# Performance work log

Measured on AMD Instinct MI355X. Metric: run time of the kernel, lower is better.

## Reference

```python
import jax, jax.numpy as jnp
import numpy as np

B, N, D = 4, 2048, 768
OUT = 768

def setup_inputs() -> dict:
    key = jax.random.key(0)
    k1, k2 = jax.random.split(key)
    x = jax.random.normal(k1, (B, N, D), dtype=jnp.float32)
    kernel = jax.random.normal(k2, (3, D, OUT), dtype=jnp.float32) * 0.02
    return {"x": x, "kernel": kernel}

def reference(x, kernel):
    # Single-head attention with shared QKV kernel stack [3, D, OUT]
    q = jnp.einsum('bnd,do->bno', x, kernel[0])
    k = jnp.einsum('bnd,do->bno', x, kernel[1])
    v = jnp.einsum('bnd,do->bno', x, kernel[2])
    # NOTE: original divides by 64**0.5 == 8 regardless of dims (faithful)
    scores = jnp.einsum('bqo,bko->bqk', q, k) / 8.0
    attn = jax.nn.softmax(scores, axis=-1)
    return jnp.einsum('bqk,bko->bqo', attn, v)
```

## Files before the change

### kernel.cpp

```cpp
#include <hip/hip_runtime.h>
#include <hip/hip_bf16.h>

constexpr int B_ = 4, N_ = 2048, D_ = 768, OUT_ = 768;
constexpr int M_ = B_ * N_;

typedef __attribute__((ext_vector_type(8))) short short8;
typedef __attribute__((ext_vector_type(4))) float floatx4;

__device__ __forceinline__ unsigned short f2bfu(float f) {
    union { __hip_bfloat16 b; unsigned short u; } cv;
    cv.b = __float2bfloat16(f);
    return cv.u;
}

#define GLOAD_LDS16(g, l)                                                     \
    __builtin_amdgcn_global_load_lds(                                         \
        (const __attribute__((address_space(1))) void*)(g),                   \
        (__attribute__((address_space(3))) void*)(l), 16, 0, 0)

#define MFMA_BF16 __builtin_amdgcn_mfma_f32_16x16x32_bf16
#define SBAR __builtin_amdgcn_s_barrier
#define SCHED0 __builtin_amdgcn_sched_barrier

template <int MFR, int NT>
__device__ __forceinline__ void gemm_tb(
    const __hip_bfloat16* __restrict__ aG, int lda,
    const __hip_bfloat16* __restrict__ bG, int ldb,
    unsigned short* LDS, floatx4 (&acc)[MFR][4]) {
    constexpr int BSLOT = (MFR == 4) ? 8192 : 4096;
    constexpr int BUFS = 4096 + BSLOT;
    constexpr int LOADS = (MFR == 4) ? 3 : 2;
    const int tid = threadIdx.x;
    const int wave = tid >> 6, lane = tid & 63;
    const int lr = lane & 15, kq = lane >> 4;
    const int wm = (MFR == 4) ? (wave >> 2) * 64 : (wave >> 1) * 32;
    const int wn = (MFR == 4) ? (wave & 3) * 64 : (wave & 1) * 64;

    const int p0 = tid >> 3, g0 = (tid & 7) ^ (p0 & 7);
    const __hip_bfloat16* pa =
        aG + (size_t)(2 * p0 + (g0 >> 2)) * lda + (g0 & 3) * 8;
    const __hip_bfloat16* pb0 =
        bG + (size_t)(2 * p0 + (g0 >> 2)) * ldb + (g0 & 3) * 8;
    const __hip_bfloat16* pb1 = bG;
    if constexpr (MFR == 4) {
        const int u = 512 + tid, p1 = u >> 3, g1 = (u & 7) ^ (p1 & 7);
        pb1 = bG + (size_t)(2 * p1 + (g1 >> 2)) * ldb + (g1 & 3) * 8;
    }

    int oa[MFR], ob[4];
#pragma unroll
    for (int mi = 0; mi < MFR; ++mi) {
        const int r = wm + mi * 16 + lr, p = r >> 1;
        const int g = ((r & 1) << 2) | kq;
        oa[mi] = p * 64 + ((g ^ (p & 7)) * 8);
    }
#pragma unroll
    for (int ni = 0; ni < 4; ++ni) {
        const int r = wn + ni * 16 + lr, p = r >> 1;
        const int g = ((r & 1) << 2) | kq;
        ob[ni] = p * 64 + ((g ^ (p & 7)) * 8);
    }

    auto STAGE = [&](int tt, int buf) {
        unsigned short* d = LDS + buf * BUFS + wave * 512;
        GLOAD_LDS16(pa + tt * 32, d);
        GLOAD_LDS16(pb0 + tt * 32, d + 4096);
        if constexpr (MFR == 4) GLOAD_LDS16(pb1 + tt * 32, d + 8192);
    };

    STAGE(0, 0);
    STAGE(1, 1);
    asm volatile("s_waitcnt vmcnt(%0)" ::"i"(LOADS) : "memory");
    SBAR();
    SCHED0(0);

    int bR = 0, bS = 2;
    for (int t = 0; t < NT; ++t) {
        const unsigned short* Ab = LDS + bR * BUFS;
        const unsigned short* Bb = Ab + 4096;
        short8 af[MFR], bf[4];
#pragma unroll
        for (int mi = 0; mi < MFR; ++mi)
            af[mi] = *(const short8*)(Ab + oa[mi]);
#pragma unroll
        for (int ni = 0; ni < 4; ++ni)
            bf[ni] = *(const short8*)(Bb + ob[ni]);
        if (t + 2 < NT) STAGE(t + 2, bS);
#pragma unroll
        for (int mi = 0; mi < MFR; ++mi)
#pragma unroll
            for (int ni = 0; ni < 4; ++ni)
                acc[mi][ni] = MFMA_BF16(af[mi], bf[ni], acc[mi][ni], 0, 0, 0);
        if (t + 2 < NT)
            asm volatile("s_waitcnt vmcnt(%0)" ::"i"(LOADS) : "memory");
        else if (t + 1 < NT)
            asm volatile("s_waitcnt vmcnt(0)" ::: "memory");
        if (t + 1 < NT) {
            SBAR();
            SCHED0(0);
        }
        bR = (bR == 2) ? 0 : bR + 1;
        bS = (bS == 2) ? 0 : bS + 1;
    }
}

__global__ __launch_bounds__(256)
void prep(const float* __restrict__ x, const float* __restrict__ w,
          __hip_bfloat16* __restrict__ xb, __hip_bfloat16* __restrict__ wt,
          float* __restrict__ l) {
    __shared__ float t[32][33];
    const int tid = threadIdx.x;
    if (blockIdx.x < 3072) {
        const size_t i = (size_t)blockIdx.x * 2048 + (size_t)tid * 8;
        float4 a = *(const float4*)(x + i);
        float4 b = *(const float4*)(x + i + 4);
        *(ushort4*)((unsigned short*)xb + i) =
            make_ushort4(f2bfu(a.x), f2bfu(a.y), f2bfu(a.z), f2bfu(a.w));
        *(ushort4*)((unsigned short*)xb + i + 4) =
            make_ushort4(f2bfu(b.x), f2bfu(b.y), f2bfu(b.z), f2bfu(b.w));
    } else if (blockIdx.x < 4800) {
        const int bid = blockIdx.x - 3072;
        const int s = bid / 576, rem = bid % 576;
        const int d0 = (rem / 24) * 32, o0 = (rem % 24) * 32;
        const int tx = tid & 31, ty = tid >> 5;
        const float* ws = w + (size_t)s * D_ * OUT_;
        __hip_bfloat16* wts = wt + (size_t)s * OUT_ * D_;
#pragma unroll
        for (int i = 0; i < 4; ++i)
            t[ty + 8 * i][tx] = ws[(size_t)(d0 + ty + 8 * i) * OUT_ + o0 + tx];
        __syncthreads();
#pragma unroll
        for (int i = 0; i < 4; ++i)
            wts[(size_t)(o0 + ty + 8 * i) * D_ + d0 + tx] =
                __float2bfloat16(t[tx][ty + 8 * i]);
    } else {
        float4* l4 = (float4*)l;
#pragma unroll
        for (int i = 0; i < 8; ++i) l4[i * 256 + tid] = make_float4(0, 0, 0, 0);
    }
}

__global__ __launch_bounds__(512, 4)
void qkv_mfma(const __hip_bfloat16* __restrict__ xb,
              const __hip_bfloat16* __restrict__ wt,
              __hip_bfloat16* __restrict__ q, __hip_bfloat16* __restrict__ k,
              __hip_bfloat16* __restrict__ vt) {
    __shared__ __align__(16) unsigned short LDS[36864];
    const int s = blockIdx.z;
    const int m0 = blockIdx.x * 128, n0 = blockIdx.y * 256;
    floatx4 acc[4][4] = {};
    gemm_tb<4, 24>(xb + (size_t)m0 * D_, D_,
                   wt + (size_t)s * OUT_ * D_ + (size_t)n0 * D_, D_, LDS, acc);

    const int tid = threadIdx.x, wave = tid >> 6, lane = tid & 63;
    const int lrow = lane & 15, kq = lane >> 4;
    const int wm = (wave >> 2) * 64, wn = (wave & 3) * 64;
    unsigned short* E = LDS;

    if (s < 2) {
        __syncthreads();
#pragma unroll
        for (int mi = 0; mi < 4; ++mi)
#pragma unroll
            for (int ni = 0; ni < 4; ++ni) {
                const int n = wn + ni * 16 + lrow;
#pragma unroll
                for (int r = 0; r < 4; ++r)
                    E[(wm + mi * 16 + kq * 4 + r) * 264 + n] =
                        f2bfu(acc[mi][ni][r]);
            }
        __syncthreads();
        unsigned short* outp = (unsigned short*)(s == 0 ? q : k);
#pragma unroll
        for (int i = 0; i < 8; ++i) {
            const int u = i * 512 + tid, row = u >> 5, c = u & 31;
            *(short8*)(outp + (size_t)(m0 + row) * OUT_ + n0 + c * 8) =
                *(const short8*)(E + row * 264 + c * 8);
        }
    } else {
        __syncthreads();
#pragma unroll
        for (int mi = 0; mi < 4; ++mi)
#pragma unroll
            for (int ni = 0; ni < 4; ++ni) {
                const int n = wn + ni * 16 + lrow;
#pragma unroll
                for (int r = 0; r < 4; ++r)
                    E[n * 136 + wm + mi * 16 + kq * 4 + r] =
                        f2bfu(acc[mi][ni][r]);
            }
        __syncthreads();
        const int b = m0 >> 11, j0 = m0 & 2047;
#pragma unroll
        for (int i = 0; i < 8; ++i) {
            const int u = i * 512 + tid, nr = u >> 4, c = u & 15;
            *(short8*)((unsigned short*)vt + ((size_t)b * OUT_ + n0 + nr) * N_ +
                       j0 + c * 8) = *(const short8*)(E + nr * 136 + c * 8);
        }
    }
}

__global__ __launch_bounds__(512, 4)
void scores_mfma(const __hip_bfloat16* __restrict__ q,
                 const __hip_bfloat16* __restrict__ k,
                 __hip_bfloat16* __restrict__ pt, float* __restrict__ l) {
    __shared__ __align__(16) unsigned short LDS[36864];
    const int b = blockIdx.z;
    const int m0 = blockIdx.x * 128, n0 = blockIdx.y * 256;
    floatx4 acc[4][4] = {};
    gemm_tb<4, 24>(q + (size_t)b * N_ * OUT_ + (size_t)m0 * OUT_, OUT_,
                   k + (size_t)b * N_ * OUT_ + (size_t)n0 * OUT_, OUT_, LDS,
                   acc);

    const int tid = threadIdx.x, wave = tid >> 6, lane = tid & 63;
    const int lrow = lane & 15, kq = lane >> 4;
    const int wm = (wave >> 2) * 64, wn = (wave & 3) * 64;

    float rs[4][4];
#pragma unroll
    for (int mi = 0; mi < 4; ++mi)
#pragma unroll
        for (int r = 0; r < 4; ++r) rs[mi][r] = 0.0f;
#pragma unroll
    for (int mi = 0; mi < 4; ++mi)
#pragma unroll
        for (int ni = 0; ni < 4; ++ni)
#pragma unroll
            for (int r = 0; r < 4; ++r) {
                const float e = __expf(acc[mi][ni][r] * 0.125f - 8.0f);
                acc[mi][ni][r] = e;
                rs[mi][r] += e;
            }
#pragma unroll
    for (int mi = 0; mi < 4; ++mi)
#pragma unroll
        for (int r = 0; r < 4; ++r) {
            float v = rs[mi][r];
            v += __shfl_xor(v, 1, 64);
            v += __shfl_xor(v, 2, 64);
            v += __shfl_xor(v, 4, 64);
            v += __shfl_xor(v, 8, 64);
            if (lrow == 0)
                atomicAdd(&l[(size_t)b * N_ + m0 + wm + mi * 16 + kq * 4 + r],
                          v);
        }

    unsigned short* E = LDS;
    unsigned short* pb = (unsigned short*)pt + (size_t)b * N_ * N_;
    __syncthreads();
#pragma unroll
    for (int mi = 0; mi < 4; ++mi)
#pragma unroll
        for (int ni = 0; ni < 4; ++ni) {
            const int n = wn + ni * 16 + lrow;
#pragma unroll
            for (int r = 0; r < 4; ++r)
                E[(wm + mi * 16 + kq * 4 + r) * 258 + n] =
                    f2bfu(acc[mi][ni][r]);
        }
    __syncthreads();
#pragma unroll
    for (int i = 0; i < 8; ++i) {
        const int u = i * 512 + tid, row = u >> 5, c = u & 31;
        *(short8*)(pb + (size_t)(m0 + row) * N_ + n0 + c * 8) =
            *(const short8*)(E + row * 258 + c * 8);
    }
}

__global__ __launch_bounds__(512, 4)
void pv_mfma(const __hip_bfloat16* __restrict__ pt,
             const __hip_bfloat16* __restrict__ vt,
             const float* __restrict__ l, float* __restrict__ out) {
    __shared__ __align__(16) unsigned short LDS[24576];
    const int b = blockIdx.z;
    const int m0 = blockIdx.x * 128, n0 = blockIdx.y * 128;
    floatx4 acc[2][4] = {};
    gemm_tb<2, 64>(pt + (size_t)b * N_ * N_ + (size_t)m0 * N_, N_,
                   vt + (size_t)b * OUT_ * N_ + (size_t)n0 * N_, N_, LDS, acc);

    const int tid = threadIdx.x, wave = tid >> 6, lane = tid & 63;
    const int lrow = lane & 15, kq = lane >> 4;
    const int wm = (wave >> 1) * 32, wn = (wave & 1) * 64;
    const float* lb = l + (size_t)b * N_ + m0 + wm;
#pragma unroll
    for (int mi = 0; mi < 2; ++mi)
#pragma unroll
        for (int r = 0; r < 4; ++r) {
            const float inv = 1.0f / lb[mi * 16 + kq * 4 + r];
            float* o = out +
                       ((size_t)b * N_ + m0 + wm + mi * 16 + kq * 4 + r) *
                           OUT_ +
                       n0 + wn;
#pragma unroll
            for (int ni = 0; ni < 4; ++ni)
                o[ni * 16 + lrow] = acc[mi][ni][r] * inv;
        }
}

extern "C" void kernel_launch(void* const* d_in, const int* in_sizes, int n_in,
                              void* d_out, int out_size, void* d_ws,
                              size_t ws_size, hipStream_t stream) {
    const float* x = (const float*)d_in[0];
    const float* w = (const float*)d_in[1];
    float* out = (float*)d_out;

    __hip_bfloat16* q  = (__hip_bfloat16*)d_ws;
    __hip_bfloat16* k  = q + (size_t)M_ * OUT_;
    __hip_bfloat16* vt = k + (size_t)M_ * OUT_;
    __hip_bfloat16* xb = vt + (size_t)M_ * OUT_;
    __hip_bfloat16* wt = xb + (size_t)M_ * D_;
    float* l = (float*)(wt + (size_t)3 * OUT_ * D_);
    __hip_bfloat16* pt = (__hip_bfloat16*)(l + M_);

    prep<<<dim3(4801), dim3(256), 0, stream>>>(x, w, xb, wt, l);
    qkv_mfma<<<dim3(64, 3, 3), dim3(512), 0, stream>>>(xb, wt, q, k, vt);
    scores_mfma<<<dim3(16, 8, 4), dim3(512), 0, stream>>>(q, k, pt, l);
    pv_mfma<<<dim3(16, 6, 4), dim3(512), 0, stream>>>(pt, vt, l, out);
}
```

Before: 189.7 us.

## Switch GEMMs to double-buffered LDS, halve epilogue staging, retile PV kernel

Replaces the triple-buffered LDS pipeline with a double-buffered one that issues the next tile's loads before the current tile's MFMAs, and raises MFMA wave priority with s_setprio. Epilogues now stage output in two halves so each kernel needs less LDS, which allows six blocks per CU instead of four in the QKV and scores kernels. The PV kernel moves to 256-thread blocks with 64x256 tiles and a 4x4 accumulator per wave. The aim is more resident waves to hide latency, at the cost of shallower prefetch and an extra barrier pair in each epilogue.

```diff
diff --git a/kernel.cpp b/kernel.cpp
--- a/kernel.cpp
+++ b/kernel.cpp
@@ -21,86 +21,79 @@
 #define MFMA_BF16 __builtin_amdgcn_mfma_f32_16x16x32_bf16
 #define SBAR __builtin_amdgcn_s_barrier
 #define SCHED0 __builtin_amdgcn_sched_barrier
-
-template <int MFR, int NT>
-__device__ __forceinline__ void gemm_tb(
+#define PRIO __builtin_amdgcn_s_setprio
+
+template <int THREADS, int NT>
+__device__ __forceinline__ void gemm_db(
     const __hip_bfloat16* __restrict__ aG, int lda,
     const __hip_bfloat16* __restrict__ bG, int ldb,
-    unsigned short* LDS, floatx4 (&acc)[MFR][4]) {
-    constexpr int BSLOT = (MFR == 4) ? 8192 : 4096;
-    constexpr int BUFS = 4096 + BSLOT;
-    constexpr int LOADS = (MFR == 4) ? 3 : 2;
+    unsigned short* LDS, floatx4 (&acc)[4][4]) {
+    constexpr int NB = (THREADS == 512) ? 2 : 4;
+    constexpr int BBASE = (THREADS == 512) ? 4096 : 2048;
+    constexpr int BUFS = BBASE + 8192;
     const int tid = threadIdx.x;
     const int wave = tid >> 6, lane = tid & 63;
     const int lr = lane & 15, kq = lane >> 4;
-    const int wm = (MFR == 4) ? (wave >> 2) * 64 : (wave >> 1) * 32;
-    const int wn = (MFR == 4) ? (wave & 3) * 64 : (wave & 1) * 64;
+    const int wm = (THREADS == 512) ? (wave >> 2) * 64 : 0;
+    const int wn = (THREADS == 512) ? (wave & 3) * 64 : wave * 64;
 
     const int p0 = tid >> 3, g0 = (tid & 7) ^ (p0 & 7);
     const __hip_bfloat16* pa =
         aG + (size_t)(2 * p0 + (g0 >> 2)) * lda + (g0 & 3) * 8;
-    const __hip_bfloat16* pb0 =
-        bG + (size_t)(2 * p0 + (g0 >> 2)) * ldb + (g0 & 3) * 8;
-    const __hip_bfloat16* pb1 = bG;
-    if constexpr (MFR == 4) {
-        const int u = 512 + tid, p1 = u >> 3, g1 = (u & 7) ^ (p1 & 7);
-        pb1 = bG + (size_t)(2 * p1 + (g1 >> 2)) * ldb + (g1 & 3) * 8;
-    }
-
-    int oa[MFR], ob[4];
-#pragma unroll
-    for (int mi = 0; mi < MFR; ++mi) {
-        const int r = wm + mi * 16 + lr, p = r >> 1;
-        const int g = ((r & 1) << 2) | kq;
-        oa[mi] = p * 64 + ((g ^ (p & 7)) * 8);
-    }
-#pragma unroll
-    for (int ni = 0; ni < 4; ++ni) {
-        const int r = wn + ni * 16 + lr, p = r >> 1;
-        const int g = ((r & 1) << 2) | kq;
-        ob[ni] = p * 64 + ((g ^ (p & 7)) * 8);
+    const __hip_bfloat16* pb[NB];
+#pragma unroll
+    for (int j = 0; j < NB; ++j) {
+        const int u = j * THREADS + tid, p = u >> 3, g = (u & 7) ^ (p & 7);
+        pb[j] = bG + (size_t)(2 * p + (g >> 2)) * ldb + (g & 3) * 8;
+    }
+
+    int oa[4], ob[4];
+#pragma unroll
+    for (int i = 0; i < 4; ++i) {
+        const int ra = wm + i * 16 + lr, pA = ra >> 1;
+        const int gA = ((ra & 1) << 2) | kq;
+        oa[i] = pA * 64 + ((gA ^ (pA & 7)) * 8);
+        const int rb = wn + i * 16 + lr, pB = rb >> 1;
+        const int gB = ((rb & 1) << 2) | kq;
+        ob[i] = pB * 64 + ((gB ^ (pB & 7)) * 8);
     }
 
     auto STAGE = [&](int tt, int buf) {
         unsigned short* d = LDS + buf * BUFS + wave * 512;
         GLOAD_LDS16(pa + tt * 32, d);
-        GLOAD_LDS16(pb0 + tt * 32, d + 4096);
-        if constexpr (MFR == 4) GLOAD_LDS16(pb1 + tt * 32, d + 8192);
+#pragma unroll
+        for (int j = 0; j < NB; ++j)
+            GLOAD_LDS16(pb[j] + tt * 32, d + BBASE + j * (THREADS * 8));
     };
 
     STAGE(0, 0);
-    STAGE(1, 1);
-    asm volatile("s_waitcnt vmcnt(%0)" ::"i"(LOADS) : "memory");
+    asm volatile("s_waitcnt vmcnt(0)" ::: "memory");
     SBAR();
     SCHED0(0);
 
-    int bR = 0, bS = 2;
     for (int t = 0; t < NT; ++t) {
-        const unsigned short* Ab = LDS + bR * BUFS;
-        const unsigned short* Bb = Ab + 4096;
-        short8 af[MFR], bf[4];
-#pragma unroll
-        for (int mi = 0; mi < MFR; ++mi)
+        if (t + 1 < NT) STAGE(t + 1, (t + 1) & 1);
+        const unsigned short* Ab = LDS + (t & 1) * BUFS;
+        const unsigned short* Bb = Ab + BBASE;
+        short8 af[4], bf[4];
+#pragma unroll
+        for (int mi = 0; mi < 4; ++mi)
             af[mi] = *(const short8*)(Ab + oa[mi]);
 #pragma unroll
         for (int ni = 0; ni < 4; ++ni)
             bf[ni] = *(const short8*)(Bb + ob[ni]);
-        if (t + 2 < NT) STAGE(t + 2, bS);
-#pragma unroll
-        for (int mi = 0; mi < MFR; ++mi)
+        PRIO(1);
+#pragma unroll
+        for (int mi = 0; mi < 4; ++mi)
 #pragma unroll
             for (int ni = 0; ni < 4; ++ni)
                 acc[mi][ni] = MFMA_BF16(af[mi], bf[ni], acc[mi][ni], 0, 0, 0);
-        if (t + 2 < NT)
-            asm volatile("s_waitcnt vmcnt(%0)" ::"i"(LOADS) : "memory");
-        else if (t + 1 < NT)
+        PRIO(0);
+        if (t + 1 < NT) {
             asm volatile("s_waitcnt vmcnt(0)" ::: "memory");
-        if (t + 1 < NT) {
             SBAR();
             SCHED0(0);
         }
-        bR = (bR == 2) ? 0 : bR + 1;
-        bS = (bS == 2) ? 0 : bS + 1;
     }
 }
 
@@ -140,17 +133,18 @@
     }
 }
 
-__global__ __launch_bounds__(512, 4)
+__global__ __launch_bounds__(512, 6)
 void qkv_mfma(const __hip_bfloat16* __restrict__ xb,
               const __hip_bfloat16* __restrict__ wt,
               __hip_bfloat16* __restrict__ q, __hip_bfloat16* __restrict__ k,
               __hip_bfloat16* __restrict__ vt) {
-    __shared__ __align__(16) unsigned short LDS[36864];
+    __shared__ __align__(16) unsigned short LDS[24576];
     const int s = blockIdx.z;
     const int m0 = blockIdx.x * 128, n0 = blockIdx.y * 256;
     floatx4 acc[4][4] = {};
-    gemm_tb<4, 24>(xb + (size_t)m0 * D_, D_,
-                   wt + (size_t)s * OUT_ * D_ + (size_t)n0 * D_, D_, LDS, acc);
+    gemm_db<512, 24>(xb + (size_t)m0 * D_, D_,
+                     wt + (size_t)s * OUT_ * D_ + (size_t)n0 * D_, D_, LDS,
+                     acc);
 
     const int tid = threadIdx.x, wave = tid >> 6, lane = tid & 63;
     const int lrow = lane & 15, kq = lane >> 4;
@@ -158,59 +152,70 @@
     unsigned short* E = LDS;
 
     if (s < 2) {
-        __syncthreads();
-#pragma unroll
-        for (int mi = 0; mi < 4; ++mi)
-#pragma unroll
-            for (int ni = 0; ni < 4; ++ni) {
-                const int n = wn + ni * 16 + lrow;
-#pragma unroll
-                for (int r = 0; r < 4; ++r)
-                    E[(wm + mi * 16 + kq * 4 + r) * 264 + n] =
-                        f2bfu(acc[mi][ni][r]);
-            }
-        __syncthreads();
         unsigned short* outp = (unsigned short*)(s == 0 ? q : k);
 #pragma unroll
-        for (int i = 0; i < 8; ++i) {
-            const int u = i * 512 + tid, row = u >> 5, c = u & 31;
-            *(short8*)(outp + (size_t)(m0 + row) * OUT_ + n0 + c * 8) =
-                *(const short8*)(E + row * 264 + c * 8);
+        for (int h = 0; h < 2; ++h) {
+            __syncthreads();
+            if ((wave >> 2) == h) {
+#pragma unroll
+                for (int mi = 0; mi < 4; ++mi)
+#pragma unroll
+                    for (int ni = 0; ni < 4; ++ni) {
+                        const int n = wn + ni * 16 + lrow;
+#pragma unroll
+                        for (int r = 0; r < 4; ++r)
+                            E[(mi * 16 + kq * 4 + r) * 264 + n] =
+                                f2bfu(acc[mi][ni][r]);
+                    }
+            }
+            __syncthreads();
+#pragma unroll
+            for (int i = 0; i < 4; ++i) {
+                const int u = i * 512 + tid, row = u >> 5, c = u & 31;
+                *(short8*)(outp + (size_t)(m0 + h * 64 + row) * OUT_ + n0 +
+                           c * 8) = *(const short8*)(E + row * 264 + c * 8);
+            }
         }
     } else {
-        __syncthreads();
-#pragma unroll
-        for (int mi = 0; mi < 4; ++mi)
-#pragma unroll
-            for (int ni = 0; ni < 4; ++ni) {
-                const int n = wn + ni * 16 + lrow;
-#pragma unroll
-                for (int r = 0; r < 4; ++r)
-                    E[n * 136 + wm + mi * 16 + kq * 4 + r] =
-                        f2bfu(acc[mi][ni][r]);
-            }
-        __syncthreads();
         const int b = m0 >> 11, j0 = m0 & 2047;
 #pragma unroll
-        for (int i = 0; i < 8; ++i) {
-            const int u = i * 512 + tid, nr = u >> 4, c = u & 15;
-            *(short8*)((unsigned short*)vt + ((size_t)b * OUT_ + n0 + nr) * N_ +
-                       j0 + c * 8) = *(const short8*)(E + nr * 136 + c * 8);
-        }
-    }
-}
-
-__global__ __launch_bounds__(512, 4)
+        for (int h = 0; h < 2; ++h) {
+            __syncthreads();
+            if ((wn >> 7) == h) {
+#pragma unroll
+                for (int mi = 0; mi < 4; ++mi)
+#pragma unroll
+                    for (int ni = 0; ni < 4; ++ni) {
+                        const int nl = (wn & 127) + ni * 16 + lrow;
+#pragma unroll
+                        for (int r = 0; r < 4; ++r)
+                            E[nl * 136 + wm + mi * 16 + kq * 4 + r] =
+                                f2bfu(acc[mi][ni][r]);
+                    }
+            }
+            __syncthreads();
+#pragma unroll
+            for (int i = 0; i < 4; ++i) {
+                const int u = i * 512 + tid, nr = u >> 4, c = u & 15;
+                *(short8*)((unsigned short*)vt +
+                           ((size_t)b * OUT_ + n0 + h * 128 + nr) * N_ + j0 +
+                           c * 8) = *(const short8*)(E + nr * 136 + c * 8);
+            }
+        }
+    }
+}
+
+__global__ __launch_bounds__(512, 6)
 void scores_mfma(const __hip_bfloat16* __restrict__ q,
                  const __hip_bfloat16* __restrict__ k,
                  __hip_bfloat16* __restrict__ pt, float* __restrict__ l) {
-    __shared__ __align__(16) unsigned short LDS[36864];
+    __shared__ __align__(16) unsigned short LDS[24576];
     const int b = blockIdx.z;
     const int m0 = blockIdx.x * 128, n0 = blockIdx.y * 256;
     floatx4 acc[4][4] = {};
-    gemm_tb<4, 24>(q + (size_t)b * N_ * OUT_ + (size_t)m0 * OUT_, OUT_,
-                   k + (size_t)b * N_ * OUT_ + (size_t)n0 * OUT_, OUT_, LDS,
-                   acc);
+    gemm_db<512, 24>(q + (size_t)b * N_ * OUT_ + (size_t)m0 * OUT_, OUT_,
+                     k + (size_t)b * N_ * OUT_ + (size_t)n0 * OUT_, OUT_, LDS,
+                     acc);
 
     const int tid = threadIdx.x, wave = tid >> 6, lane = tid & 63;
     const int lrow = lane & 15, kq = lane >> 4;
@@ -247,50 +252,55 @@
 
     unsigned short* E = LDS;
     unsigned short* pb = (unsigned short*)pt + (size_t)b * N_ * N_;
-    __syncthreads();
-#pragma unroll
-    for (int mi = 0; mi < 4; ++mi)
-#pragma unroll
-        for (int ni = 0; ni < 4; ++ni) {
-            const int n = wn + ni * 16 + lrow;
-#pragma unroll
-            for (int r = 0; r < 4; ++r)
-                E[(wm + mi * 16 + kq * 4 + r) * 258 + n] =
-                    f2bfu(acc[mi][ni][r]);
-        }
-    __syncthreads();
-#pragma unroll
-    for (int i = 0; i < 8; ++i) {
-        const int u = i * 512 + tid, row = u >> 5, c = u & 31;
-        *(short8*)(pb + (size_t)(m0 + row) * N_ + n0 + c * 8) =
-            *(const short8*)(E + row * 258 + c * 8);
-    }
-}
-
-__global__ __launch_bounds__(512, 4)
+#pragma unroll
+    for (int h = 0; h < 2; ++h) {
+        __syncthreads();
+        if ((wave >> 2) == h) {
+#pragma unroll
+            for (int mi = 0; mi < 4; ++mi)
+#pragma unroll
+                for (int ni = 0; ni < 4; ++ni) {
+                    const int n = wn + ni * 16 + lrow;
+#pragma unroll
+                    for (int r = 0; r < 4; ++r)
+                        E[(mi * 16 + kq * 4 + r) * 258 + n] =
+                            f2bfu(acc[mi][ni][r]);
+                }
+        }
+        __syncthreads();
+#pragma unroll
+        for (int i = 0; i < 4; ++i) {
+            const int u = i * 512 + tid, row = u >> 5, c = u & 31;
+            *(short8*)(pb + (size_t)(m0 + h * 64 + row) * N_ + n0 + c * 8) =
+                *(const short8*)(E + row * 258 + c * 8);
+        }
+    }
+}
+
+__global__ __launch_bounds__(256, 4)
 void pv_mfma(const __hip_bfloat16* __restrict__ pt,
              const __hip_bfloat16* __restrict__ vt,
              const float* __restrict__ l, float* __restrict__ out) {
-    __shared__ __align__(16) unsigned short LDS[24576];
+    __shared__ __align__(16) unsigned short LDS[20480];
     const int b = blockIdx.z;
-    const int m0 = blockIdx.x * 128, n0 = blockIdx.y * 128;
-    floatx4 acc[2][4] = {};
-    gemm_tb<2, 64>(pt + (size_t)b * N_ * N_ + (size_t)m0 * N_, N_,
-                   vt + (size_t)b * OUT_ * N_ + (size_t)n0 * N_, N_, LDS, acc);
+    const int m0 = blockIdx.x * 64, n0 = blockIdx.y * 256;
+    floatx4 acc[4][4] = {};
+    gemm_db<256, 64>(pt + (size_t)b * N_ * N_ + (size_t)m0 * N_, N_,
+                     vt + (size_t)b * OUT_ * N_ + (size_t)n0 * N_, N_, LDS,
+                     acc);
 
     const int tid = threadIdx.x, wave = tid >> 6, lane = tid & 63;
     const int lrow = lane & 15, kq = lane >> 4;
-    const int wm = (wave >> 1) * 32, wn = (wave & 1) * 64;
-    const float* lb = l + (size_t)b * N_ + m0 + wm;
-#pragma unroll
-    for (int mi = 0; mi < 2; ++mi)
+    const int wn = wave * 64;
+    const float* lb = l + (size_t)b * N_ + m0;
+#pragma unroll
+    for (int mi = 0; mi < 4; ++mi)
 #pragma unroll
         for (int r = 0; r < 4; ++r) {
-            const float inv = 1.0f / lb[mi * 16 + kq * 4 + r];
-            float* o = out +
-                       ((size_t)b * N_ + m0 + wm + mi * 16 + kq * 4 + r) *
-                           OUT_ +
-                       n0 + wn;
+            const int row = mi * 16 + kq * 4 + r;
+            const float inv = 1.0f / lb[row];
+            float* o =
+                out + ((size_t)b * N_ + m0 + row) * OUT_ + n0 + wn;
 #pragma unroll
             for (int ni = 0; ni < 4; ++ni)
                 o[ni * 16 + lrow] = acc[mi][ni][r] * inv;
@@ -315,5 +325,5 @@
     prep<<<dim3(4801), dim3(256), 0, stream>>>(x, w, xb, wt, l);
     qkv_mfma<<<dim3(64, 3, 3), dim3(512), 0, stream>>>(xb, wt, q, k, vt);
     scores_mfma<<<dim3(16, 8, 4), dim3(512), 0, stream>>>(q, k, pt, l);
-    pv_mfma<<<dim3(16, 6, 4), dim3(512), 0, stream>>>(pt, vt, l, out);
-}
+    pv_mfma<<<dim3(32, 3, 4), dim3(256), 0, stream>>>(pt, vt, l, out);
+}
```

Measured after the change: 527.7 us. 178% more time.

## Use 256x256 block tiles with split-phase MFMA pipeline for QKV and scores GEMMs

Applied to the files above, without the earlier changes.

The QKV and scores GEMMs move from 128x256 to 256x256 block tiles, with each wave computing a 128x64 sub-tile. The main loop is split into two MFMA phases that interleave the A and B global-to-LDS stages, and it raises wave priority with s_setprio around the MFMA bursts. The aim is to cut global and LDS traffic per FLOP and overlap loads with math better. In exchange the accumulators double, occupancy drops to 2 blocks per SM, and the grids shrink to 288 and 256 blocks, which may underfill the 256 CUs.

```diff
diff --git a/kernel.cpp b/kernel.cpp
--- a/kernel.cpp
+++ b/kernel.cpp
@@ -21,56 +21,149 @@
 #define MFMA_BF16 __builtin_amdgcn_mfma_f32_16x16x32_bf16
 #define SBAR __builtin_amdgcn_s_barrier
 #define SCHED0 __builtin_amdgcn_sched_barrier
-
-template <int MFR, int NT>
-__device__ __forceinline__ void gemm_tb(
+#define PRIO __builtin_amdgcn_s_setprio
+#define WAIT_LGKM0 asm volatile("s_waitcnt lgkmcnt(0)" ::: "memory")
+
+template <int NT>
+__device__ __forceinline__ void gemm8p(
     const __hip_bfloat16* __restrict__ aG, int lda,
     const __hip_bfloat16* __restrict__ bG, int ldb,
-    unsigned short* LDS, floatx4 (&acc)[MFR][4]) {
-    constexpr int BSLOT = (MFR == 4) ? 8192 : 4096;
-    constexpr int BUFS = 4096 + BSLOT;
-    constexpr int LOADS = (MFR == 4) ? 3 : 2;
+    unsigned short* LDS, floatx4 (&acc)[8][4]) {
     const int tid = threadIdx.x;
     const int wave = tid >> 6, lane = tid & 63;
     const int lr = lane & 15, kq = lane >> 4;
-    const int wm = (MFR == 4) ? (wave >> 2) * 64 : (wave >> 1) * 32;
-    const int wn = (MFR == 4) ? (wave & 3) * 64 : (wave & 1) * 64;
+    const int wm = (wave >> 2) * 128, wn = (wave & 3) * 64;
 
     const int p0 = tid >> 3, g0 = (tid & 7) ^ (p0 & 7);
     const __hip_bfloat16* pa =
         aG + (size_t)(2 * p0 + (g0 >> 2)) * lda + (g0 & 3) * 8;
-    const __hip_bfloat16* pb0 =
+    const __hip_bfloat16* pb =
         bG + (size_t)(2 * p0 + (g0 >> 2)) * ldb + (g0 & 3) * 8;
-    const __hip_bfloat16* pb1 = bG;
-    if constexpr (MFR == 4) {
-        const int u = 512 + tid, p1 = u >> 3, g1 = (u & 7) ^ (p1 & 7);
-        pb1 = bG + (size_t)(2 * p1 + (g1 >> 2)) * ldb + (g1 & 3) * 8;
-    }
-
-    int oa[MFR], ob[4];
-#pragma unroll
-    for (int mi = 0; mi < MFR; ++mi) {
-        const int r = wm + mi * 16 + lr, p = r >> 1;
+    const size_t a1 = (size_t)128 * lda, b1 = (size_t)128 * ldb;
+
+    int Aoff[8], Boff[4];
+#pragma unroll
+    for (int mi = 0; mi < 8; ++mi) {
+        const int r = mi * 16 + lr, p = r >> 1;
         const int g = ((r & 1) << 2) | kq;
-        oa[mi] = p * 64 + ((g ^ (p & 7)) * 8);
+        Aoff[mi] = (wm >> 7) * 4096 + p * 64 + ((g ^ (p & 7)) * 8);
     }
 #pragma unroll
     for (int ni = 0; ni < 4; ++ni) {
-        const int r = wn + ni * 16 + lr, p = r >> 1;
+        const int r = (wn & 64) + ni * 16 + lr, p = r >> 1;
         const int g = ((r & 1) << 2) | kq;
-        ob[ni] = p * 64 + ((g ^ (p & 7)) * 8);
+        Boff[ni] = 8192 + (wn >> 7) * 4096 + p * 64 + ((g ^ (p & 7)) * 8);
+    }
+
+#define STG_A(kt, S)                                                         \
+    do {                                                                     \
+        unsigned short* d_ = LDS + (S) + wave * 512;                         \
+        GLOAD_LDS16(pa + (kt) * 32, d_);                                     \
+        GLOAD_LDS16(pa + a1 + (kt) * 32, d_ + 4096);                         \
+    } while (0)
+#define STG_B(kt, S)                                                         \
+    do {                                                                     \
+        unsigned short* d_ = LDS + (S) + 8192 + wave * 512;                  \
+        GLOAD_LDS16(pb + (kt) * 32, d_);                                     \
+        GLOAD_LDS16(pb + b1 + (kt) * 32, d_ + 4096);                         \
+    } while (0)
+
+    STG_A(0, 0); STG_B(0, 0);
+    STG_A(1, 16384); STG_B(1, 16384);
+    asm volatile("s_waitcnt vmcnt(4)" ::: "memory");
+    SBAR();
+    SCHED0(0);
+
+    int rb = 0, sb = 2;
+    for (int t = 0; t < NT; ++t) {
+        const unsigned short* Q = LDS + rb * 16384;
+        const int S = sb * 16384;
+        short8 af[4], bf[4];
+#pragma unroll
+        for (int i = 0; i < 4; ++i) af[i] = *(const short8*)(Q + Aoff[i]);
+#pragma unroll
+        for (int i = 0; i < 4; ++i) bf[i] = *(const short8*)(Q + Boff[i]);
+        if (t + 2 < NT) STG_A(t + 2, S);
+        SBAR();
+        WAIT_LGKM0;
+        SCHED0(0);
+        PRIO(1);
+#pragma unroll
+        for (int mi = 0; mi < 4; ++mi)
+#pragma unroll
+            for (int ni = 0; ni < 4; ++ni)
+                acc[mi][ni] = MFMA_BF16(af[mi], bf[ni], acc[mi][ni], 0, 0, 0);
+        PRIO(0);
+        SBAR();
+#pragma unroll
+        for (int i = 0; i < 4; ++i) af[i] = *(const short8*)(Q + Aoff[4 + i]);
+        if (t + 2 < NT) STG_B(t + 2, S);
+        SBAR();
+        WAIT_LGKM0;
+        SCHED0(0);
+        PRIO(1);
+#pragma unroll
+        for (int mi = 0; mi < 4; ++mi)
+#pragma unroll
+            for (int ni = 0; ni < 4; ++ni)
+                acc[4 + mi][ni] =
+                    MFMA_BF16(af[mi], bf[ni], acc[4 + mi][ni], 0, 0, 0);
+        PRIO(0);
+        if (t + 2 < NT)
+            asm volatile("s_waitcnt vmcnt(4)" ::: "memory");
+        else if (t + 1 < NT)
+            asm volatile("s_waitcnt vmcnt(0)" ::: "memory");
+        if (t + 1 < NT) {
+            SBAR();
+            SCHED0(0);
+        }
+        rb = (rb == 2) ? 0 : rb + 1;
+        sb = (sb == 2) ? 0 : sb + 1;
+    }
+#undef STG_A
+#undef STG_B
+}
+
+template <int NT>
+__device__ __forceinline__ void gemm_tb2(
+    const __hip_bfloat16* __restrict__ aG, int lda,
+    const __hip_bfloat16* __restrict__ bG, int ldb,
+    unsigned short* LDS, floatx4 (&acc)[2][4]) {
+    constexpr int BUFS = 4096 + 4096;
+    const int tid = threadIdx.x;
+    const int wave = tid >> 6, lane = tid & 63;
+    const int lr = lane & 15, kq = lane >> 4;
+    const int wm = (wave >> 1) * 32, wn = (wave & 1) * 64;
+
+    const int p0 = tid >> 3, g0 = (tid & 7) ^ (p0 & 7);
+    const __hip_bfloat16* pa =
+        aG + (size_t)(2 * p0 + (g0 >> 2)) * lda + (g0 & 3) * 8;
+    const __hip_bfloat16* pb =
+        bG + (size_t)(2 * p0 + (g0 >> 2)) * ldb + (g0 & 3) * 8;
+
+    int oa[2], ob[4];
+#pragma unroll
+    for (int i = 0; i < 2; ++i) {
+        const int ra = wm + i * 16 + lr, p = ra >> 1;
+        const int g = ((ra & 1) << 2) | kq;
+        oa[i] = p * 64 + ((g ^ (p & 7)) * 8);
+    }
+#pragma unroll
+    for (int i = 0; i < 4; ++i) {
+        const int rbw = wn + i * 16 + lr, p = rbw >> 1;
+        const int g = ((rbw & 1) << 2) | kq;
+        ob[i] = p * 64 + ((g ^ (p & 7)) * 8);
     }
 
     auto STAGE = [&](int tt, int buf) {
         unsigned short* d = LDS + buf * BUFS + wave * 512;
         GLOAD_LDS16(pa + tt * 32, d);
-        GLOAD_LDS16(pb0 + tt * 32, d + 4096);
-        if constexpr (MFR == 4) GLOAD_LDS16(pb1 + tt * 32, d + 8192);
+        GLOAD_LDS16(pb + tt * 32, d + 4096);
     };
 
     STAGE(0, 0);
     STAGE(1, 1);
-    asm volatile("s_waitcnt vmcnt(%0)" ::"i"(LOADS) : "memory");
+    asm volatile("s_waitcnt vmcnt(2)" ::: "memory");
     SBAR();
     SCHED0(0);
 
@@ -78,21 +171,19 @@
     for (int t = 0; t < NT; ++t) {
         const unsigned short* Ab = LDS + bR * BUFS;
         const unsigned short* Bb = Ab + 4096;
-        short8 af[MFR], bf[4];
-#pragma unroll
-        for (int mi = 0; mi < MFR; ++mi)
-            af[mi] = *(const short8*)(Ab + oa[mi]);
-#pragma unroll
-        for (int ni = 0; ni < 4; ++ni)
-            bf[ni] = *(const short8*)(Bb + ob[ni]);
+        short8 af[2], bf[4];
+#pragma unroll
+        for (int mi = 0; mi < 2; ++mi) af[mi] = *(const short8*)(Ab + oa[mi]);
+#pragma unroll
+        for (int ni = 0; ni < 4; ++ni) bf[ni] = *(const short8*)(Bb + ob[ni]);
         if (t + 2 < NT) STAGE(t + 2, bS);
 #pragma unroll
-        for (int mi = 0; mi < MFR; ++mi)
+        for (int mi = 0; mi < 2; ++mi)
 #pragma unroll
             for (int ni = 0; ni < 4; ++ni)
                 acc[mi][ni] = MFMA_BF16(af[mi], bf[ni], acc[mi][ni], 0, 0, 0);
         if (t + 2 < NT)
-            asm volatile("s_waitcnt vmcnt(%0)" ::"i"(LOADS) : "memory");
+            asm volatile("s_waitcnt vmcnt(2)" ::: "memory");
         else if (t + 1 < NT)
             asm volatile("s_waitcnt vmcnt(0)" ::: "memory");
         if (t + 1 < NT) {
@@ -140,89 +231,99 @@
     }
 }
 
-__global__ __launch_bounds__(512, 4)
+__global__ __launch_bounds__(512, 2)
 void qkv_mfma(const __hip_bfloat16* __restrict__ xb,
               const __hip_bfloat16* __restrict__ wt,
               __hip_bfloat16* __restrict__ q, __hip_bfloat16* __restrict__ k,
               __hip_bfloat16* __restrict__ vt) {
-    __shared__ __align__(16) unsigned short LDS[36864];
+    __shared__ __align__(16) unsigned short LDS[49152];
     const int s = blockIdx.z;
-    const int m0 = blockIdx.x * 128, n0 = blockIdx.y * 256;
-    floatx4 acc[4][4] = {};
-    gemm_tb<4, 24>(xb + (size_t)m0 * D_, D_,
-                   wt + (size_t)s * OUT_ * D_ + (size_t)n0 * D_, D_, LDS, acc);
+    const int m0 = blockIdx.x * 256, n0 = blockIdx.y * 256;
+    floatx4 acc[8][4] = {};
+    gemm8p<24>(xb + (size_t)m0 * D_, D_,
+               wt + (size_t)s * OUT_ * D_ + (size_t)n0 * D_, D_, LDS, acc);
 
     const int tid = threadIdx.x, wave = tid >> 6, lane = tid & 63;
     const int lrow = lane & 15, kq = lane >> 4;
-    const int wm = (wave >> 2) * 64, wn = (wave & 3) * 64;
+    const int wm = (wave >> 2) * 128, wn = (wave & 3) * 64;
     unsigned short* E = LDS;
 
     if (s < 2) {
-        __syncthreads();
-#pragma unroll
-        for (int mi = 0; mi < 4; ++mi)
-#pragma unroll
-            for (int ni = 0; ni < 4; ++ni) {
-                const int n = wn + ni * 16 + lrow;
-#pragma unroll
-                for (int r = 0; r < 4; ++r)
-                    E[(wm + mi * 16 + kq * 4 + r) * 264 + n] =
-                        f2bfu(acc[mi][ni][r]);
+        unsigned short* outp = (unsigned short*)(s == 0 ? q : k);
+#pragma unroll
+        for (int h = 0; h < 2; ++h) {
+            __syncthreads();
+            if ((wm >> 7) == h) {
+#pragma unroll
+                for (int mi = 0; mi < 8; ++mi)
+#pragma unroll
+                    for (int ni = 0; ni < 4; ++ni) {
+                        const int n = wn + ni * 16 + lrow;
+#pragma unroll
+                        for (int r = 0; r < 4; ++r)
+                            E[(mi * 16 + kq * 4 + r) * 264 + n] =
+                                f2bfu(acc[mi][ni][r]);
+                    }
             }
-        __syncthreads();
-        unsigned short* outp = (unsigned short*)(s == 0 ? q : k);
-#pragma unroll
-        for (int i = 0; i < 8; ++i) {
-            const int u = i * 512 + tid, row = u >> 5, c = u & 31;
-            *(short8*)(outp + (size_t)(m0 + row) * OUT_ + n0 + c * 8) =
-                *(const short8*)(E + row * 264 + c * 8);
+            __syncthreads();
+#pragma unroll
+            for (int i = 0; i < 8; ++i) {
+                const int u = i * 512 + tid, row = u >> 5, c = u & 31;
+                *(short8*)(outp + (size_t)(m0 + h * 128 + row) * OUT_ + n0 +
+                           c * 8) = *(const short8*)(E + row * 264 + c * 8);
+            }
         }
     } else {
-        __syncthreads();
-#pragma unroll
-        for (int mi = 0; mi < 4; ++mi)
-#pragma unroll
-            for (int ni = 0; ni < 4; ++ni) {
-                const int n = wn + ni * 16 + lrow;
-#pragma unroll
-                for (int r = 0; r < 4; ++r)
-                    E[n * 136 + wm + mi * 16 + kq * 4 + r] =
-                        f2bfu(acc[mi][ni][r]);
+        const int b = m0 >> 11, j0 = m0 & 2047;
+#pragma unroll
+        for (int h = 0; h < 2; ++h) {
+            __syncthreads();
+            if ((wn >> 7) == h) {
+#pragma unroll
+                for (int mi = 0; mi < 8; ++mi)
+#pragma unroll
+                    for (int ni = 0; ni < 4; ++ni) {
+                        const int nl = (wn & 64) + ni * 16 + lrow;
+#pragma unroll
+                        for (int r = 0; r < 4; ++r)
+                            E[nl * 264 + wm + mi * 16 + kq * 4 + r] =
+                                f2bfu(acc[mi][ni][r]);
+                    }
             }
-        __syncthreads();
-        const int b = m0 >> 11, j0 = m0 & 2047;
-#pragma unroll
-        for (int i = 0; i < 8; ++i) {
-            const int u = i * 512 + tid, nr = u >> 4, c = u & 15;
-            *(short8*)((unsigned short*)vt + ((size_t)b * OUT_ + n0 + nr) * N_ +
-                       j0 + c * 8) = *(const short8*)(E + nr * 136 + c * 8);
-        }
-    }
-}
-
-__global__ __launch_bounds__(512, 4)
+            __syncthreads();
+#pragma unroll
+            for (int i = 0; i < 8; ++i) {
+                const int u = i * 512 + tid, nr = u >> 5, c = u & 31;
+                *(short8*)((unsigned short*)vt +
+                           ((size_t)b * OUT_ + n0 + h * 128 + nr) * N_ + j0 +
+                           c * 8) = *(const short8*)(E + nr * 264 + c * 8);
+            }
+        }
+    }
+}
+
+__global__ __launch_bounds__(512, 2)
 void scores_mfma(const __hip_bfloat16* __restrict__ q,
                  const __hip_bfloat16* __restrict__ k,
                  __hip_bfloat16* __restrict__ pt, float* __restrict__ l) {
-    __shared__ __align__(16) unsigned short LDS[36864];
+    __shared__ __align__(16) unsigned short LDS[49152];
     const int b = blockIdx.z;
-    const int m0 = blockIdx.x * 128, n0 = blockIdx.y * 256;
-    floatx4 acc[4][4] = {};
-    gemm_tb<4, 24>(q + (size_t)b * N_ * OUT_ + (size_t)m0 * OUT_, OUT_,
-                   k + (size_t)b * N_ * OUT_ + (size_t)n0 * OUT_, OUT_, LDS,
-                   acc);
+    const int m0 = blockIdx.x * 256, n0 = blockIdx.y * 256;
+    floatx4 acc[8][4] = {};
+    gemm8p<24>(q + (size_t)b * N_ * OUT_ + (size_t)m0 * OUT_, OUT_,
+               k + (size_t)b * N_ * OUT_ + (size_t)n0 * OUT_, OUT_, LDS, acc);
 
     const int tid = threadIdx.x, wave = tid >> 6, lane = tid & 63;
     const int lrow = lane & 15, kq = lane >> 4;
-    const int wm = (wave >> 2) * 64, wn = (wave & 3) * 64;
-
-    float rs[4][4];
-#pragma unroll
-    for (int mi = 0; mi < 4; ++mi)
+    const int wm = (wave >> 2) * 128, wn = (wave & 3) * 64;
+
+    float rs[8][4];
+#pragma unroll
+    for (int mi = 0; mi < 8; ++mi)
 #pragma unroll
         for (int r = 0; r < 4; ++r) rs[mi][r] = 0.0f;
 #pragma unroll
-    for (int mi = 0; mi < 4; ++mi)
+    for (int mi = 0; mi < 8; ++mi)
 #pragma unroll
         for (int ni = 0; ni < 4; ++ni)
 #pragma unroll
@@ -232,7 +333,7 @@
                 rs[mi][r] += e;
             }
 #pragma unroll
-    for (int mi = 0; mi < 4; ++mi)
+    for (int mi = 0; mi < 8; ++mi)
 #pragma unroll
         for (int r = 0; r < 4; ++r) {
             float v = rs[mi][r];
@@ -247,23 +348,28 @@
 
     unsigned short* E = LDS;
     unsigned short* pb = (unsigned short*)pt + (size_t)b * N_ * N_;
-    __syncthreads();
-#pragma unroll
-    for (int mi = 0; mi < 4; ++mi)
-#pragma unroll
-        for (int ni = 0; ni < 4; ++ni) {
-            const int n = wn + ni * 16 + lrow;
-#pragma unroll
-            for (int r = 0; r < 4; ++r)
-                E[(wm + mi * 16 + kq * 4 + r) * 258 + n] =
-                    f2bfu(acc[mi][ni][r]);
-        }
-    __syncthreads();
-#pragma unroll
-    for (int i = 0; i < 8; ++i) {
-        const int u = i * 512 + tid, row = u >> 5, c = u & 31;
-        *(short8*)(pb + (size_t)(m0 + row) * N_ + n0 + c * 8) =
-            *(const short8*)(E + row * 258 + c * 8);
+#pragma unroll
+    for (int h = 0; h < 2; ++h) {
+        __syncthreads();
+        if ((wm >> 7) == h) {
+#pragma unroll
+            for (int mi = 0; mi < 8; ++mi)
+#pragma unroll
+                for (int ni = 0; ni < 4; ++ni) {
+                    const int n = wn + ni * 16 + lrow;
+#pragma unroll
+                    for (int r = 0; r < 4; ++r)
+                        E[(mi * 16 + kq * 4 + r) * 258 + n] =
+                            f2bfu(acc[mi][ni][r]);
+                }
+        }
+        __syncthreads();
+#pragma unroll
+        for (int i = 0; i < 8; ++i) {
+            const int u = i * 512 + tid, row = u >> 5, c = u & 31;
+            *(short8*)(pb + (size_t)(m0 + h * 128 + row) * N_ + n0 + c * 8) =
+                *(const short8*)(E + row * 258 + c * 8);
+        }
     }
 }
 
@@ -275,8 +381,8 @@
     const int b = blockIdx.z;
     const int m0 = blockIdx.x * 128, n0 = blockIdx.y * 128;
     floatx4 acc[2][4] = {};
-    gemm_tb<2, 64>(pt + (size_t)b * N_ * N_ + (size_t)m0 * N_, N_,
-                   vt + (size_t)b * OUT_ * N_ + (size_t)n0 * N_, N_, LDS, acc);
+    gemm_tb2<64>(pt + (size_t)b * N_ * N_ + (size_t)m0 * N_, N_,
+                 vt + (size_t)b * OUT_ * N_ + (size_t)n0 * N_, N_, LDS, acc);
 
     const int tid = threadIdx.x, wave = tid >> 6, lane = tid & 63;
     const int lrow = lane & 15, kq = lane >> 4;
@@ -313,7 +419,7 @@
     __hip_bfloat16* pt = (__hip_bfloat16*)(l + M_);
 
     prep<<<dim3(4801), dim3(256), 0, stream>>>(x, w, xb, wt, l);
-    qkv_mfma<<<dim3(64, 3, 3), dim3(512), 0, stream>>>(xb, wt, q, k, vt);
-    scores_mfma<<<dim3(16, 8, 4), dim3(512), 0, stream>>>(q, k, pt, l);
+    qkv_mfma<<<dim3(32, 3, 3), dim3(512), 0, stream>>>(xb, wt, q, k, vt);
+    scores_mfma<<<dim3(8, 8, 4), dim3(512), 0, stream>>>(q, k, pt, l);
     pv_mfma<<<dim3(16, 6, 4), dim3(512), 0, stream>>>(pt, vt, l, out);
 }
```

New measurement: 200.4 us. 1.06x slower.

## Unify all GEMMs on a 128x128 tile with four waves

Applied to the files above, without the earlier changes.

Replaces the two gemm_tb variants (128x256 with 8 waves, and 128x128 with 8 waves of 2x4 fragments) with a single 128x128 tile computed by 4 waves, each holding a 4x4 MFMA fragment block. Grids double for the qkv and scores kernels, launch bounds drop to 256 threads, and LDS and epilogue strides shrink to match. The aim is more blocks for better CU load balance, and in pv more MFMA work per LDS fragment load. The cost is less operand reuse per block in qkv/scores and fewer waves per block to hide latency.

```diff
diff --git a/kernel.cpp b/kernel.cpp
--- a/kernel.cpp
+++ b/kernel.cpp
@@ -22,77 +22,68 @@
 #define SBAR __builtin_amdgcn_s_barrier
 #define SCHED0 __builtin_amdgcn_sched_barrier
 
-template <int MFR, int NT>
-__device__ __forceinline__ void gemm_tb(
+template <int NT>
+__device__ __forceinline__ void gemm128(
     const __hip_bfloat16* __restrict__ aG, int lda,
     const __hip_bfloat16* __restrict__ bG, int ldb,
-    unsigned short* LDS, floatx4 (&acc)[MFR][4]) {
-    constexpr int BSLOT = (MFR == 4) ? 8192 : 4096;
-    constexpr int BUFS = 4096 + BSLOT;
-    constexpr int LOADS = (MFR == 4) ? 3 : 2;
+    unsigned short* LDS, floatx4 (&acc)[4][4]) {
     const int tid = threadIdx.x;
     const int wave = tid >> 6, lane = tid & 63;
     const int lr = lane & 15, kq = lane >> 4;
-    const int wm = (MFR == 4) ? (wave >> 2) * 64 : (wave >> 1) * 32;
-    const int wn = (MFR == 4) ? (wave & 3) * 64 : (wave & 1) * 64;
+    const int wm = (wave >> 1) * 64, wn = (wave & 1) * 64;
 
     const int p0 = tid >> 3, g0 = (tid & 7) ^ (p0 & 7);
-    const __hip_bfloat16* pa =
+    const int u1 = 256 + tid, p1 = u1 >> 3, g1 = (u1 & 7) ^ (p1 & 7);
+    const __hip_bfloat16* pa0 =
         aG + (size_t)(2 * p0 + (g0 >> 2)) * lda + (g0 & 3) * 8;
+    const __hip_bfloat16* pa1 =
+        aG + (size_t)(2 * p1 + (g1 >> 2)) * lda + (g1 & 3) * 8;
     const __hip_bfloat16* pb0 =
         bG + (size_t)(2 * p0 + (g0 >> 2)) * ldb + (g0 & 3) * 8;
-    const __hip_bfloat16* pb1 = bG;
-    if constexpr (MFR == 4) {
-        const int u = 512 + tid, p1 = u >> 3, g1 = (u & 7) ^ (p1 & 7);
-        pb1 = bG + (size_t)(2 * p1 + (g1 >> 2)) * ldb + (g1 & 3) * 8;
-    }
-
-    int oa[MFR], ob[4];
-#pragma unroll
-    for (int mi = 0; mi < MFR; ++mi) {
-        const int r = wm + mi * 16 + lr, p = r >> 1;
-        const int g = ((r & 1) << 2) | kq;
-        oa[mi] = p * 64 + ((g ^ (p & 7)) * 8);
-    }
-#pragma unroll
-    for (int ni = 0; ni < 4; ++ni) {
-        const int r = wn + ni * 16 + lr, p = r >> 1;
-        const int g = ((r & 1) << 2) | kq;
-        ob[ni] = p * 64 + ((g ^ (p & 7)) * 8);
+    const __hip_bfloat16* pb1 =
+        bG + (size_t)(2 * p1 + (g1 >> 2)) * ldb + (g1 & 3) * 8;
+
+    int oa[4], ob[4];
+#pragma unroll
+    for (int i = 0; i < 4; ++i) {
+        const int ra = wm + i * 16 + lr, pA = ra >> 1;
+        const int gA = ((ra & 1) << 2) | kq;
+        oa[i] = pA * 64 + ((gA ^ (pA & 7)) * 8);
+        const int rb = wn + i * 16 + lr, pB = rb >> 1;
+        const int gB = ((rb & 1) << 2) | kq;
+        ob[i] = 4096 + pB * 64 + ((gB ^ (pB & 7)) * 8);
     }
 
     auto STAGE = [&](int tt, int buf) {
-        unsigned short* d = LDS + buf * BUFS + wave * 512;
-        GLOAD_LDS16(pa + tt * 32, d);
+        unsigned short* d = LDS + buf * 8192 + wave * 512;
+        GLOAD_LDS16(pa0 + tt * 32, d);
+        GLOAD_LDS16(pa1 + tt * 32, d + 2048);
         GLOAD_LDS16(pb0 + tt * 32, d + 4096);
-        if constexpr (MFR == 4) GLOAD_LDS16(pb1 + tt * 32, d + 8192);
+        GLOAD_LDS16(pb1 + tt * 32, d + 6144);
     };
 
     STAGE(0, 0);
     STAGE(1, 1);
-    asm volatile("s_waitcnt vmcnt(%0)" ::"i"(LOADS) : "memory");
+    asm volatile("s_waitcnt vmcnt(4)" ::: "memory");
     SBAR();
     SCHED0(0);
 
     int bR = 0, bS = 2;
     for (int t = 0; t < NT; ++t) {
-        const unsigned short* Ab = LDS + bR * BUFS;
-        const unsigned short* Bb = Ab + 4096;
-        short8 af[MFR], bf[4];
-#pragma unroll
-        for (int mi = 0; mi < MFR; ++mi)
-            af[mi] = *(const short8*)(Ab + oa[mi]);
-#pragma unroll
-        for (int ni = 0; ni < 4; ++ni)
-            bf[ni] = *(const short8*)(Bb + ob[ni]);
+        const unsigned short* Ab = LDS + bR * 8192;
+        short8 af[4], bf[4];
+#pragma unroll
+        for (int mi = 0; mi < 4; ++mi) af[mi] = *(const short8*)(Ab + oa[mi]);
+#pragma unroll
+        for (int ni = 0; ni < 4; ++ni) bf[ni] = *(const short8*)(Ab + ob[ni]);
         if (t + 2 < NT) STAGE(t + 2, bS);
 #pragma unroll
-        for (int mi = 0; mi < MFR; ++mi)
+        for (int mi = 0; mi < 4; ++mi)
 #pragma unroll
             for (int ni = 0; ni < 4; ++ni)
                 acc[mi][ni] = MFMA_BF16(af[mi], bf[ni], acc[mi][ni], 0, 0, 0);
         if (t + 2 < NT)
-            asm volatile("s_waitcnt vmcnt(%0)" ::"i"(LOADS) : "memory");
+            asm volatile("s_waitcnt vmcnt(4)" ::: "memory");
         else if (t + 1 < NT)
             asm volatile("s_waitcnt vmcnt(0)" ::: "memory");
         if (t + 1 < NT) {
@@ -140,25 +131,25 @@
     }
 }
 
-__global__ __launch_bounds__(512, 4)
+__global__ __launch_bounds__(256, 3)
 void qkv_mfma(const __hip_bfloat16* __restrict__ xb,
               const __hip_bfloat16* __restrict__ wt,
               __hip_bfloat16* __restrict__ q, __hip_bfloat16* __restrict__ k,
               __hip_bfloat16* __restrict__ vt) {
-    __shared__ __align__(16) unsigned short LDS[36864];
+    __shared__ __align__(16) unsigned short LDS[24576];
     const int s = blockIdx.z;
-    const int m0 = blockIdx.x * 128, n0 = blockIdx.y * 256;
+    const int m0 = blockIdx.x * 128, n0 = blockIdx.y * 128;
     floatx4 acc[4][4] = {};
-    gemm_tb<4, 24>(xb + (size_t)m0 * D_, D_,
-                   wt + (size_t)s * OUT_ * D_ + (size_t)n0 * D_, D_, LDS, acc);
+    gemm128<24>(xb + (size_t)m0 * D_, D_,
+                wt + (size_t)s * OUT_ * D_ + (size_t)n0 * D_, D_, LDS, acc);
 
     const int tid = threadIdx.x, wave = tid >> 6, lane = tid & 63;
     const int lrow = lane & 15, kq = lane >> 4;
-    const int wm = (wave >> 2) * 64, wn = (wave & 3) * 64;
+    const int wm = (wave >> 1) * 64, wn = (wave & 1) * 64;
     unsigned short* E = LDS;
+    __syncthreads();
 
     if (s < 2) {
-        __syncthreads();
 #pragma unroll
         for (int mi = 0; mi < 4; ++mi)
 #pragma unroll
@@ -166,19 +157,18 @@
                 const int n = wn + ni * 16 + lrow;
 #pragma unroll
                 for (int r = 0; r < 4; ++r)
-                    E[(wm + mi * 16 + kq * 4 + r) * 264 + n] =
+                    E[(wm + mi * 16 + kq * 4 + r) * 136 + n] =
                         f2bfu(acc[mi][ni][r]);
             }
         __syncthreads();
         unsigned short* outp = (unsigned short*)(s == 0 ? q : k);
 #pragma unroll
         for (int i = 0; i < 8; ++i) {
-            const int u = i * 512 + tid, row = u >> 5, c = u & 31;
+            const int u = i * 256 + tid, row = u >> 4, c = u & 15;
             *(short8*)(outp + (size_t)(m0 + row) * OUT_ + n0 + c * 8) =
-                *(const short8*)(E + row * 264 + c * 8);
+                *(const short8*)(E + row * 136 + c * 8);
         }
     } else {
-        __syncthreads();
 #pragma unroll
         for (int mi = 0; mi < 4; ++mi)
 #pragma unroll
@@ -193,28 +183,27 @@
         const int b = m0 >> 11, j0 = m0 & 2047;
 #pragma unroll
         for (int i = 0; i < 8; ++i) {
-            const int u = i * 512 + tid, nr = u >> 4, c = u & 15;
+            const int u = i * 256 + tid, nr = u >> 4, c = u & 15;
             *(short8*)((unsigned short*)vt + ((size_t)b * OUT_ + n0 + nr) * N_ +
                        j0 + c * 8) = *(const short8*)(E + nr * 136 + c * 8);
         }
     }
 }
 
-__global__ __launch_bounds__(512, 4)
+__global__ __launch_bounds__(256, 3)
 void scores_mfma(const __hip_bfloat16* __restrict__ q,
                  const __hip_bfloat16* __restrict__ k,
                  __hip_bfloat16* __restrict__ pt, float* __restrict__ l) {
-    __shared__ __align__(16) unsigned short LDS[36864];
+    __shared__ __align__(16) unsigned short LDS[24576];
     const int b = blockIdx.z;
-    const int m0 = blockIdx.x * 128, n0 = blockIdx.y * 256;
+    const int m0 = blockIdx.x * 128, n0 = blockIdx.y * 128;
     floatx4 acc[4][4] = {};
-    gemm_tb<4, 24>(q + (size_t)b * N_ * OUT_ + (size_t)m0 * OUT_, OUT_,
-                   k + (size_t)b * N_ * OUT_ + (size_t)n0 * OUT_, OUT_, LDS,
-                   acc);
+    gemm128<24>(q + (size_t)b * N_ * OUT_ + (size_t)m0 * OUT_, OUT_,
+                k + (size_t)b * N_ * OUT_ + (size_t)n0 * OUT_, OUT_, LDS, acc);
 
     const int tid = threadIdx.x, wave = tid >> 6, lane = tid & 63;
     const int lrow = lane & 15, kq = lane >> 4;
-    const int wm = (wave >> 2) * 64, wn = (wave & 3) * 64;
+    const int wm = (wave >> 1) * 64, wn = (wave & 1) * 64;
 
     float rs[4][4];
 #pragma unroll
@@ -255,35 +244,35 @@
             const int n = wn + ni * 16 + lrow;
 #pragma unroll
             for (int r = 0; r < 4; ++r)
-                E[(wm + mi * 16 + kq * 4 + r) * 258 + n] =
+                E[(wm + mi * 16 + kq * 4 + r) * 130 + n] =
                     f2bfu(acc[mi][ni][r]);
         }
     __syncthreads();
 #pragma unroll
     for (int i = 0; i < 8; ++i) {
-        const int u = i * 512 + tid, row = u >> 5, c = u & 31;
+        const int u = i * 256 + tid, row = u >> 4, c = u & 15;
         *(short8*)(pb + (size_t)(m0 + row) * N_ + n0 + c * 8) =
-            *(const short8*)(E + row * 258 + c * 8);
-    }
-}
-
-__global__ __launch_bounds__(512, 4)
+            *(const short8*)(E + row * 130 + c * 8);
+    }
+}
+
+__global__ __launch_bounds__(256, 3)
 void pv_mfma(const __hip_bfloat16* __restrict__ pt,
              const __hip_bfloat16* __restrict__ vt,
              const float* __restrict__ l, float* __restrict__ out) {
     __shared__ __align__(16) unsigned short LDS[24576];
     const int b = blockIdx.z;
     const int m0 = blockIdx.x * 128, n0 = blockIdx.y * 128;
-    floatx4 acc[2][4] = {};
-    gemm_tb<2, 64>(pt + (size_t)b * N_ * N_ + (size_t)m0 * N_, N_,
-                   vt + (size_t)b * OUT_ * N_ + (size_t)n0 * N_, N_, LDS, acc);
+    floatx4 acc[4][4] = {};
+    gemm128<64>(pt + (size_t)b * N_ * N_ + (size_t)m0 * N_, N_,
+                vt + (size_t)b * OUT_ * N_ + (size_t)n0 * N_, N_, LDS, acc);
 
     const int tid = threadIdx.x, wave = tid >> 6, lane = tid & 63;
     const int lrow = lane & 15, kq = lane >> 4;
-    const int wm = (wave >> 1) * 32, wn = (wave & 1) * 64;
+    const int wm = (wave >> 1) * 64, wn = (wave & 1) * 64;
     const float* lb = l + (size_t)b * N_ + m0 + wm;
 #pragma unroll
-    for (int mi = 0; mi < 2; ++mi)
+    for (int mi = 0; mi < 4; ++mi)
 #pragma unroll
         for (int r = 0; r < 4; ++r) {
             const float inv = 1.0f / lb[mi * 16 + kq * 4 + r];
@@ -313,7 +302,7 @@
     __hip_bfloat16* pt = (__hip_bfloat16*)(l + M_);
 
     prep<<<dim3(4801), dim3(256), 0, stream>>>(x, w, xb, wt, l);
-    qkv_mfma<<<dim3(64, 3, 3), dim3(512), 0, stream>>>(xb, wt, q, k, vt);
-    scores_mfma<<<dim3(16, 8, 4), dim3(512), 0, stream>>>(q, k, pt, l);
-    pv_mfma<<<dim3(16, 6, 4), dim3(512), 0, stream>>>(pt, vt, l, out);
-}
+    qkv_mfma<<<dim3(64, 6, 3), dim3(256), 0, stream>>>(xb, wt, q, k, vt);
+    scores_mfma<<<dim3(16, 16, 4), dim3(256), 0, stream>>>(q, k, pt, l);
+    pv_mfma<<<dim3(16, 6, 4), dim3(256), 0, stream>>>(pt, vt, l, out);
+}
```

Measured after the change: 196.4 us. +3.5%, slower.
